# Performance work log

Hardware: AMD Instinct MI355X
Metric: run time of the kernel (lower is better)

The kernel has to match this reference:

```python
import jax, jax.numpy as jnp
import numpy as np

N_NODES = 100000
N_EDGES = 1600000
IN_DIM, HID_DIM, OUT_DIM = 128, 64, 64


def setup_inputs() -> dict:
    key = jax.random.key(0)
    ks = jax.random.split(key, 8)
    x = jax.random.normal(ks[0], (N_NODES, IN_DIM), dtype=jnp.float32)
    edge_index = jax.random.randint(ks[1], (2, N_EDGES), 0, N_NODES, dtype=jnp.int32)
    edge_weight = jax.random.uniform(ks[2], (N_EDGES,), dtype=jnp.float32)
    # GCNConv parameters (glorot-ish init)
    w1 = jax.random.normal(ks[3], (IN_DIM, HID_DIM), dtype=jnp.float32) / np.sqrt(IN_DIM)
    b1 = jnp.zeros((HID_DIM,), dtype=jnp.float32)
    w2 = jax.random.normal(ks[4], (HID_DIM, OUT_DIM), dtype=jnp.float32) / np.sqrt(HID_DIM)
    b2 = jnp.zeros((OUT_DIM,), dtype=jnp.float32)
    return {"x": x, "edge_index": edge_index, "edge_weight": edge_weight,
            "w1": w1, "b1": b1, "w2": w2, "b2": b2}


def _gcn_conv(h, src, dst, edge_weight, w, b, n_nodes):
    # GCNConv(normalize=False): linear transform, then edge-weighted scatter-add
    # (source_to_target flow: gather from src, scatter-sum into dst), then bias.
    h = h @ w                                   # [N, out]
    msg = h[src] * edge_weight[:, None]          # [E, out] irregular gather
    agg = jax.ops.segment_sum(msg, dst, num_segments=n_nodes)  # [N, out]
    return agg + b


def reference(x, edge_index, edge_weight, w1, b1, w2, b2):
    src, dst = edge_index[0], edge_index[1]
    n = x.shape[0]
    # Dropout is identity in eval mode (training=False).
    h = _gcn_conv(x, src, dst, edge_weight, w1, b1, n)
    h = jax.nn.relu(h)
    out = _gcn_conv(h, src, dst, edge_weight, w2, b2, n)
    return out
```

## Files before the change

### kernel.cpp

```cpp
#include <hip/hip_runtime.h>
#include <hip/hip_bf16.h>


#define N_NODES 100000
#define N_EDGES 1600000
#define NB1     391
#define T1      4096
#define NT1     391
#define CAP1    4706

typedef unsigned short ushort_t;
typedef unsigned int uint_t;
typedef __attribute__((ext_vector_type(8))) short bf16x8;
typedef __attribute__((ext_vector_type(4))) float floatx4;
typedef __attribute__((ext_vector_type(8))) ushort_t ushort8v;

static __device__ __forceinline__ float bf2f(ushort_t h) {
    return __uint_as_float(((uint_t)h) << 16);
}
static __device__ __forceinline__ ushort_t f2bf(float f) {
    uint_t u = __float_as_uint(f);
    u = (u + 0x7FFF + ((u >> 16) & 1)) >> 16;
    return (ushort_t)u;
}

__global__ __launch_bounds__(512) void k_init(int* __restrict__ gcursor)
{
    int t = threadIdx.x;
    if (t < NB1) gcursor[t] = t * CAP1;
}

__global__ __launch_bounds__(512) void k_pass1(
    const int* __restrict__ src, const int* __restrict__ dst,
    const float* __restrict__ ew, int* __restrict__ gcursor,
    int2* __restrict__ recs1, int E)
{
    __shared__ int cnt[NB1], start[NB1], cursor[NB1], gb[NB1];
    __shared__ int s[512];
    __shared__ int2 stg[T1];
    __shared__ ushort_t sb[T1];
    const int t = threadIdx.x, b = blockIdx.x;

    if (t < NB1) cnt[t] = 0;
    __syncthreads();
    const int e0 = b * T1;
    const int e1 = min(E, e0 + T1);
    for (int e = e0 + t; e < e1; e += 512)
        atomicAdd(&cnt[dst[e] >> 8], 1);
    __syncthreads();
    const int v = (t < NB1) ? cnt[t] : 0;
    s[t] = v;
    #pragma unroll
    for (int off = 1; off < 512; off <<= 1) {
        __syncthreads();
        int a = (t >= off) ? s[t - off] : 0;
        __syncthreads();
        s[t] += a;
    }
    __syncthreads();
    if (t < NB1) {
        int st = s[t] - v;
        start[t]  = st;
        cursor[t] = st;
        gb[t]     = atomicAdd(&gcursor[t], v);
    }
    __syncthreads();
    for (int e = e0 + t; e < e1; e += 512) {
        int d  = dst[e];
        int bk = d >> 8;
        int p  = atomicAdd(&cursor[bk], 1);
        int2 r;
        r.x = ((d & 255) << 17) | src[e];
        r.y = __float_as_int(ew[e]);
        stg[p] = r;
        sb[p]  = (ushort_t)bk;
    }
    __syncthreads();
    const int n = e1 - e0;
    for (int i = t; i < n; i += 512) {
        int bk = sb[i];
        recs1[gb[bk] + (i - start[bk])] = stg[i];
    }
}

__global__ __launch_bounds__(256) void k_pass2(
    const int2* __restrict__ recs1, const int* __restrict__ gcursor,
    int2* __restrict__ recs2, int2* __restrict__ nodeinfo, int N)
{
    __shared__ int cnt[256];
    __shared__ int s[256];
    __shared__ int cursor[256];
    const int t = threadIdx.x, b = blockIdx.x;
    const int lo = b * CAP1;
    const int hi = gcursor[b];

    cnt[t] = 0;
    __syncthreads();
    for (int j = lo + t; j < hi; j += 256)
        atomicAdd(&cnt[((uint_t)recs1[j].x) >> 17], 1);
    __syncthreads();
    const int v = cnt[t];
    s[t] = v;
    #pragma unroll
    for (int off = 1; off < 256; off <<= 1) {
        __syncthreads();
        int a = (t >= off) ? s[t - off] : 0;
        __syncthreads();
        s[t] += a;
    }
    __syncthreads();
    const int stl = s[t] - v;
    cursor[t] = stl;
    const int ng = b * 256 + t;
    if (ng < N) {
        int2 ni; ni.x = lo + stl; ni.y = v;
        nodeinfo[ng] = ni;
    }
    __syncthreads();
    for (int j = lo + t; j < hi; j += 256) {
        int2 r = recs1[j];
        int dl = ((uint_t)r.x) >> 17;
        int p  = atomicAdd(&cursor[dl], 1);
        int2 o;
        o.x = r.x & 0x1FFFF;
        o.y = r.y;
        recs2[lo + p] = o;
    }
}

__global__ __launch_bounds__(256) void k_gemm1(
    const float* __restrict__ X, const float* __restrict__ W,
    ushort_t* __restrict__ Y, int N)
{
    __shared__ ushort_t sA[64 * 136];
    __shared__ ushort_t sB[64 * 136];
    const int tid  = threadIdx.x;
    const int row0 = blockIdx.x * 64;

    for (int i = tid; i < 64 * 32; i += 256) {
        int r = i >> 5, c4 = (i & 31) * 4;
        int rg = row0 + r; if (rg > N - 1) rg = N - 1;
        float4 v = *(const float4*)(X + (size_t)rg * 128 + c4);
        ushort4 pk = make_ushort4(f2bf(v.x), f2bf(v.y), f2bf(v.z), f2bf(v.w));
        *(ushort4*)(sA + r * 136 + c4) = pk;
    }
    for (int i = tid; i < 128 * 16; i += 256) {
        int k = i >> 4, n4 = (i & 15) * 4;
        float4 v = *(const float4*)(W + (size_t)k * 64 + n4);
        sB[(n4 + 0) * 136 + k] = f2bf(v.x);
        sB[(n4 + 1) * 136 + k] = f2bf(v.y);
        sB[(n4 + 2) * 136 + k] = f2bf(v.z);
        sB[(n4 + 3) * 136 + k] = f2bf(v.w);
    }
    __syncthreads();

    const int wid = tid >> 6, lane = tid & 63;
    const int m = lane & 15, quad = lane >> 4;
    floatx4 acc[4] = {};

    #pragma unroll
    for (int ks = 0; ks < 4; ++ks) {
        bf16x8 a = *(const bf16x8*)(sA + (wid * 16 + m) * 136 + ks * 32 + quad * 8);
        #pragma unroll
        for (int nt = 0; nt < 4; ++nt) {
            bf16x8 bfr = *(const bf16x8*)(sB + (nt * 16 + m) * 136 + ks * 32 + quad * 8);
            acc[nt] = __builtin_amdgcn_mfma_f32_16x16x32_bf16(a, bfr, acc[nt], 0, 0, 0);
        }
    }
    __syncthreads();
    #pragma unroll
    for (int nt = 0; nt < 4; ++nt)
        #pragma unroll
        for (int r = 0; r < 4; ++r)
            sA[(wid * 16 + quad * 4 + r) * 72 + nt * 16 + m] = f2bf(acc[nt][r]);
    __syncthreads();
    for (int i = tid; i < 64 * 8; i += 256) {
        int rr = i >> 3, c8 = (i & 7) * 8;
        int rg = row0 + rr;
        if (rg < N)
            *(ushort8v*)(Y + (size_t)rg * 64 + c8) =
                *(const ushort8v*)(sA + rr * 72 + c8);
    }
}

__global__ __launch_bounds__(256) void k_gemm2(
    const ushort_t* __restrict__ X, const float* __restrict__ W,
    ushort_t* __restrict__ Y, int N)
{
    __shared__ ushort_t sA[64 * 72];
    __shared__ ushort_t sB[64 * 72];
    const int tid  = threadIdx.x;
    const int row0 = blockIdx.x * 64;

    for (int i = tid; i < 64 * 16; i += 256) {
        int r = i >> 4, c4 = (i & 15) * 4;
        int rg = row0 + r; if (rg > N - 1) rg = N - 1;
        *(ushort4*)(sA + r * 72 + c4) =
            *(const ushort4*)(X + (size_t)rg * 64 + c4);
    }
    for (int i = tid; i < 64 * 16; i += 256) {
        int k = i >> 4, n4 = (i & 15) * 4;
        float4 v = *(const float4*)(W + (size_t)k * 64 + n4);
        sB[(n4 + 0) * 72 + k] = f2bf(v.x);
        sB[(n4 + 1) * 72 + k] = f2bf(v.y);
        sB[(n4 + 2) * 72 + k] = f2bf(v.z);
        sB[(n4 + 3) * 72 + k] = f2bf(v.w);
    }
    __syncthreads();

    const int wid = tid >> 6, lane = tid & 63;
    const int m = lane & 15, quad = lane >> 4;
    floatx4 acc[4] = {};

    #pragma unroll
    for (int ks = 0; ks < 2; ++ks) {
        bf16x8 a = *(const bf16x8*)(sA + (wid * 16 + m) * 72 + ks * 32 + quad * 8);
        #pragma unroll
        for (int nt = 0; nt < 4; ++nt) {
            bf16x8 bfr = *(const bf16x8*)(sB + (nt * 16 + m) * 72 + ks * 32 + quad * 8);
            acc[nt] = __builtin_amdgcn_mfma_f32_16x16x32_bf16(a, bfr, acc[nt], 0, 0, 0);
        }
    }
    __syncthreads();
    #pragma unroll
    for (int nt = 0; nt < 4; ++nt)
        #pragma unroll
        for (int r = 0; r < 4; ++r)
            sA[(wid * 16 + quad * 4 + r) * 72 + nt * 16 + m] = f2bf(acc[nt][r]);
    __syncthreads();
    for (int i = tid; i < 64 * 8; i += 256) {
        int rr = i >> 3, c8 = (i & 7) * 8;
        int rg = row0 + rr;
        if (rg < N)
            *(ushort8v*)(Y + (size_t)rg * 64 + c8) =
                *(const ushort8v*)(sA + rr * 72 + c8);
    }
}

template<bool RELU, bool OUT_BF16>
__global__ __launch_bounds__(256) void k_gather(
    const ushort_t* __restrict__ H, const int2* __restrict__ recs,
    const int2* __restrict__ nodeinfo, const float* __restrict__ bias,
    void* __restrict__ out)
{
    const int wid  = threadIdx.x >> 6;
    const int lane = threadIdx.x & 63;
    const int n0   = (blockIdx.x * 4 + wid) * 2;
    const int n1   = n0 + 1;

    const int2 niA = nodeinfo[n0];
    const int2 niB = nodeinfo[n1];
    int baseA = niA.x; const int endA = niA.x + niA.y;
    int baseB = niB.x; const int endB = niB.x + niB.y;

    const int g  = lane >> 4;
    const int c4 = (lane & 15) * 4;

    float a0 = 0.f, a1 = 0.f, a2 = 0.f, a3 = 0.f;
    float b0 = 0.f, b1 = 0.f, b2 = 0.f, b3 = 0.f;

    while (baseA < endA || baseB < endB) {
        int mA = endA - baseA; if (mA > 64) mA = 64;
        int mB = endB - baseB; if (mB > 64) mB = 64;
        int2 rA = (mA > 0) ? recs[baseA + (lane < mA ? lane : mA - 1)]
                           : make_int2(0, 0);
        int2 rB = (mB > 0) ? recs[baseB + (lane < mB ? lane : mB - 1)]
                           : make_int2(0, 0);
        float wAf = __int_as_float(rA.y);
        float wBf = __int_as_float(rB.y);
        int mm = mA > mB ? mA : mB;
        #pragma unroll 2
        for (int jj = 0; jj < mm; jj += 4) {
            int idx = jj + g;
            int   sA = __shfl(rA.x, idx);
            float wA = __shfl(wAf, idx);
            int   sB = __shfl(rB.x, idx);
            float wB = __shfl(wBf, idx);
            if (idx >= mA) wA = 0.f;
            if (idx >= mB) wB = 0.f;
            ushort4 hA = *(const ushort4*)(H + (size_t)sA * 64 + c4);
            ushort4 hB = *(const ushort4*)(H + (size_t)sB * 64 + c4);
            a0 = fmaf(wA, bf2f(hA.x), a0);
            a1 = fmaf(wA, bf2f(hA.y), a1);
            a2 = fmaf(wA, bf2f(hA.z), a2);
            a3 = fmaf(wA, bf2f(hA.w), a3);
            b0 = fmaf(wB, bf2f(hB.x), b0);
            b1 = fmaf(wB, bf2f(hB.y), b1);
            b2 = fmaf(wB, bf2f(hB.z), b2);
            b3 = fmaf(wB, bf2f(hB.w), b3);
        }
        baseA += 64;
        baseB += 64;
    }
    a0 += __shfl_down(a0, 32); a1 += __shfl_down(a1, 32);
    a2 += __shfl_down(a2, 32); a3 += __shfl_down(a3, 32);
    b0 += __shfl_down(b0, 32); b1 += __shfl_down(b1, 32);
    b2 += __shfl_down(b2, 32); b3 += __shfl_down(b3, 32);
    a0 += __shfl_down(a0, 16); a1 += __shfl_down(a1, 16);
    a2 += __shfl_down(a2, 16); a3 += __shfl_down(a3, 16);
    b0 += __shfl_down(b0, 16); b1 += __shfl_down(b1, 16);
    b2 += __shfl_down(b2, 16); b3 += __shfl_down(b3, 16);

    if (lane < 16) {
        float4 bv = *(const float4*)(bias + c4);
        float vA0 = a0 + bv.x, vA1 = a1 + bv.y, vA2 = a2 + bv.z, vA3 = a3 + bv.w;
        float vB0 = b0 + bv.x, vB1 = b1 + bv.y, vB2 = b2 + bv.z, vB3 = b3 + bv.w;
        if (RELU) {
            vA0 = fmaxf(vA0, 0.f); vA1 = fmaxf(vA1, 0.f);
            vA2 = fmaxf(vA2, 0.f); vA3 = fmaxf(vA3, 0.f);
            vB0 = fmaxf(vB0, 0.f); vB1 = fmaxf(vB1, 0.f);
            vB2 = fmaxf(vB2, 0.f); vB3 = fmaxf(vB3, 0.f);
        }
        if (OUT_BF16) {
            *(ushort4*)((ushort_t*)out + (size_t)n0 * 64 + c4) =
                make_ushort4(f2bf(vA0), f2bf(vA1), f2bf(vA2), f2bf(vA3));
            *(ushort4*)((ushort_t*)out + (size_t)n1 * 64 + c4) =
                make_ushort4(f2bf(vB0), f2bf(vB1), f2bf(vB2), f2bf(vB3));
        } else {
            *(float4*)((float*)out + (size_t)n0 * 64 + c4) =
                make_float4(vA0, vA1, vA2, vA3);
            *(float4*)((float*)out + (size_t)n1 * 64 + c4) =
                make_float4(vB0, vB1, vB2, vB3);
        }
    }
}

extern "C" void kernel_launch(void* const* d_in, const int* in_sizes, int n_in,
                              void* d_out, int out_size, void* d_ws, size_t ws_size,
                              hipStream_t stream) {
    const float* x   = (const float*)d_in[0];
    const int*   ei  = (const int*)  d_in[1];
    const float* ew  = (const float*)d_in[2];
    const float* w1  = (const float*)d_in[3];
    const float* b1  = (const float*)d_in[4];
    const float* w2  = (const float*)d_in[5];
    const float* b2  = (const float*)d_in[6];
    float* out = (float*)d_out;

    const int N = N_NODES, E = N_EDGES;
    const int* src = ei;
    const int* dst = ei + E;

    char* p = (char*)d_ws;
    ushort_t* bufA   = (ushort_t*)p;  p += (size_t)N_NODES * 64 * 2;
    int2*     recs2  = (int2*)p;      p += (size_t)NB1 * CAP1 * 8;
    int2*     recs1  = (int2*)p;
    ushort_t* bufB   = (ushort_t*)p;  p += (size_t)NB1 * CAP1 * 8;
    int*      gcur   = (int*)p;       p += 2048;
    int2*     ninfo  = (int2*)p;      p += (size_t)N_NODES * 8;

    k_init <<<1, 512, 0, stream>>>(gcur);
    k_pass1<<<NT1, 512, 0, stream>>>(src, dst, ew, gcur, recs1, E);
    k_pass2<<<NB1, 256, 0, stream>>>(recs1, gcur, recs2, ninfo, N);

    k_gemm1<<<(N + 63) / 64, 256, 0, stream>>>(x, w1, bufA, N);
    k_gather<true, true><<<N / 8, 256, 0, stream>>>(bufA, recs2, ninfo, b1, bufB);

    k_gemm2<<<(N + 63) / 64, 256, 0, stream>>>(bufB, w2, bufA, N);
    k_gather<false, false><<<N / 8, 256, 0, stream>>>(bufA, recs2, ninfo, b2, out);
}
```

Measured before the change: 246.8 us.

## Merge edge bucketing pass1 with first GEMM into one launch; widen pass2 blocks

Pass1 (edge bucketing by destination) and the first feature GEMM are independent, so they now run in one launch. Blocks below NT1 do the bucketing, and the remaining blocks run a 128-row, 512-thread version of the GEMM, with both sharing one raw shared-memory buffer. The aim is to overlap the memory-bound sort with the GEMM and drop a launch. Separately, pass2 now uses 1024-thread blocks to scan the bucket records faster, and the gather inner loop is unrolled 4 instead of 2. The risks are the larger shared-memory footprint per block and the larger GEMM tile lowering occupancy.

```diff
diff --git a/kernel.cpp b/kernel.cpp
--- a/kernel.cpp
+++ b/kernel.cpp
@@ -8,6 +8,7 @@
 #define T1      4096
 #define NT1     391
 #define CAP1    4706
+#define GB1     782
 
 typedef unsigned short ushort_t;
 typedef unsigned int uint_t;
@@ -30,60 +31,120 @@
     if (t < NB1) gcursor[t] = t * CAP1;
 }
 
-__global__ __launch_bounds__(512) void k_pass1(
+__global__ __launch_bounds__(512) void k_p1g1(
     const int* __restrict__ src, const int* __restrict__ dst,
     const float* __restrict__ ew, int* __restrict__ gcursor,
-    int2* __restrict__ recs1, int E)
-{
-    __shared__ int cnt[NB1], start[NB1], cursor[NB1], gb[NB1];
-    __shared__ int s[512];
-    __shared__ int2 stg[T1];
-    __shared__ ushort_t sb[T1];
-    const int t = threadIdx.x, b = blockIdx.x;
-
-    if (t < NB1) cnt[t] = 0;
-    __syncthreads();
-    const int e0 = b * T1;
-    const int e1 = min(E, e0 + T1);
-    for (int e = e0 + t; e < e1; e += 512)
-        atomicAdd(&cnt[dst[e] >> 8], 1);
-    __syncthreads();
-    const int v = (t < NB1) ? cnt[t] : 0;
-    s[t] = v;
-    #pragma unroll
-    for (int off = 1; off < 512; off <<= 1) {
-        __syncthreads();
-        int a = (t >= off) ? s[t - off] : 0;
-        __syncthreads();
-        s[t] += a;
-    }
-    __syncthreads();
-    if (t < NB1) {
-        int st = s[t] - v;
-        start[t]  = st;
-        cursor[t] = st;
-        gb[t]     = atomicAdd(&gcursor[t], v);
-    }
-    __syncthreads();
-    for (int e = e0 + t; e < e1; e += 512) {
-        int d  = dst[e];
-        int bk = d >> 8;
-        int p  = atomicAdd(&cursor[bk], 1);
-        int2 r;
-        r.x = ((d & 255) << 17) | src[e];
-        r.y = __float_as_int(ew[e]);
-        stg[p] = r;
-        sb[p]  = (ushort_t)bk;
-    }
-    __syncthreads();
-    const int n = e1 - e0;
-    for (int i = t; i < n; i += 512) {
-        int bk = sb[i];
-        recs1[gb[bk] + (i - start[bk])] = stg[i];
-    }
-}
-
-__global__ __launch_bounds__(256) void k_pass2(
+    int2* __restrict__ recs1, int E,
+    const float* __restrict__ X, const float* __restrict__ W,
+    ushort_t* __restrict__ Y, int N)
+{
+    __shared__ __align__(16) char smem[52224];
+    const int tid = threadIdx.x;
+
+    if (blockIdx.x < NT1) {
+        int* cnt     = (int*)smem;
+        int* start   = cnt + NB1;
+        int* cursor  = start + NB1;
+        int* gb      = cursor + NB1;
+        int* s       = (int*)(smem + 6256);
+        int2* stg    = (int2*)(smem + 8304);
+        ushort_t* sb = (ushort_t*)(smem + 41072);
+        const int t = tid, b = blockIdx.x;
+
+        if (t < NB1) cnt[t] = 0;
+        __syncthreads();
+        const int e0 = b * T1;
+        const int e1 = min(E, e0 + T1);
+        for (int e = e0 + t; e < e1; e += 512)
+            atomicAdd(&cnt[dst[e] >> 8], 1);
+        __syncthreads();
+        const int v = (t < NB1) ? cnt[t] : 0;
+        s[t] = v;
+        #pragma unroll
+        for (int off = 1; off < 512; off <<= 1) {
+            __syncthreads();
+            int a = (t >= off) ? s[t - off] : 0;
+            __syncthreads();
+            s[t] += a;
+        }
+        __syncthreads();
+        if (t < NB1) {
+            int st = s[t] - v;
+            start[t]  = st;
+            cursor[t] = st;
+            gb[t]     = atomicAdd(&gcursor[t], v);
+        }
+        __syncthreads();
+        for (int e = e0 + t; e < e1; e += 512) {
+            int d  = dst[e];
+            int bk = d >> 8;
+            int p  = atomicAdd(&cursor[bk], 1);
+            int2 r;
+            r.x = ((d & 255) << 17) | src[e];
+            r.y = __float_as_int(ew[e]);
+            stg[p] = r;
+            sb[p]  = (ushort_t)bk;
+        }
+        __syncthreads();
+        const int n = e1 - e0;
+        for (int i = t; i < n; i += 512) {
+            int bk = sb[i];
+            recs1[gb[bk] + (i - start[bk])] = stg[i];
+        }
+    } else {
+        ushort_t* sA = (ushort_t*)smem;
+        ushort_t* sB = (ushort_t*)(smem + 34816);
+        const int b    = blockIdx.x - NT1;
+        const int row0 = b * 128;
+
+        for (int i = tid; i < 128 * 32; i += 512) {
+            int r = i >> 5, c4 = (i & 31) * 4;
+            int rg = row0 + r; if (rg > N - 1) rg = N - 1;
+            float4 v = *(const float4*)(X + (size_t)rg * 128 + c4);
+            ushort4 pk = make_ushort4(f2bf(v.x), f2bf(v.y), f2bf(v.z), f2bf(v.w));
+            *(ushort4*)(sA + r * 136 + c4) = pk;
+        }
+        for (int i = tid; i < 128 * 16; i += 512) {
+            int k = i >> 4, n4 = (i & 15) * 4;
+            float4 v = *(const float4*)(W + (size_t)k * 64 + n4);
+            sB[(n4 + 0) * 136 + k] = f2bf(v.x);
+            sB[(n4 + 1) * 136 + k] = f2bf(v.y);
+            sB[(n4 + 2) * 136 + k] = f2bf(v.z);
+            sB[(n4 + 3) * 136 + k] = f2bf(v.w);
+        }
+        __syncthreads();
+
+        const int wid = tid >> 6, lane = tid & 63;
+        const int m = lane & 15, quad = lane >> 4;
+        floatx4 acc[4] = {};
+
+        #pragma unroll
+        for (int ks = 0; ks < 4; ++ks) {
+            bf16x8 a = *(const bf16x8*)(sA + (wid * 16 + m) * 136 + ks * 32 + quad * 8);
+            #pragma unroll
+            for (int nt = 0; nt < 4; ++nt) {
+                bf16x8 bfr = *(const bf16x8*)(sB + (nt * 16 + m) * 136 + ks * 32 + quad * 8);
+                acc[nt] = __builtin_amdgcn_mfma_f32_16x16x32_bf16(a, bfr, acc[nt], 0, 0, 0);
+            }
+        }
+        __syncthreads();
+        #pragma unroll
+        for (int nt = 0; nt < 4; ++nt)
+            #pragma unroll
+            for (int r = 0; r < 4; ++r)
+                sA[(wid * 16 + quad * 4 + r) * 72 + nt * 16 + m] = f2bf(acc[nt][r]);
+        __syncthreads();
+        for (int i = tid; i < 128 * 8; i += 512) {
+            int rr = i >> 3, c8 = (i & 7) * 8;
+            int rg = row0 + rr;
+            if (rg < N)
+                *(ushort8v*)(Y + (size_t)rg * 64 + c8) =
+                    *(const ushort8v*)(sA + rr * 72 + c8);
+        }
+    }
+}
+
+__global__ __launch_bounds__(1024) void k_pass2(
     const int2* __restrict__ recs1, const int* __restrict__ gcursor,
     int2* __restrict__ recs2, int2* __restrict__ nodeinfo, int N)
 {
@@ -94,30 +155,32 @@
     const int lo = b * CAP1;
     const int hi = gcursor[b];
 
-    cnt[t] = 0;
-    __syncthreads();
-    for (int j = lo + t; j < hi; j += 256)
+    if (t < 256) cnt[t] = 0;
+    __syncthreads();
+    for (int j = lo + t; j < hi; j += 1024)
         atomicAdd(&cnt[((uint_t)recs1[j].x) >> 17], 1);
     __syncthreads();
-    const int v = cnt[t];
-    s[t] = v;
+    const int v = (t < 256) ? cnt[t] : 0;
+    if (t < 256) s[t] = v;
     #pragma unroll
     for (int off = 1; off < 256; off <<= 1) {
         __syncthreads();
-        int a = (t >= off) ? s[t - off] : 0;
-        __syncthreads();
-        s[t] += a;
-    }
-    __syncthreads();
-    const int stl = s[t] - v;
-    cursor[t] = stl;
-    const int ng = b * 256 + t;
-    if (ng < N) {
-        int2 ni; ni.x = lo + stl; ni.y = v;
-        nodeinfo[ng] = ni;
-    }
-    __syncthreads();
-    for (int j = lo + t; j < hi; j += 256) {
+        int a = (t >= off && t < 256) ? s[t - off] : 0;
+        __syncthreads();
+        if (t < 256) s[t] += a;
+    }
+    __syncthreads();
+    if (t < 256) {
+        const int stl = s[t] - v;
+        cursor[t] = stl;
+        const int ng = b * 256 + t;
+        if (ng < N) {
+            int2 ni; ni.x = lo + stl; ni.y = v;
+            nodeinfo[ng] = ni;
+        }
+    }
+    __syncthreads();
+    for (int j = lo + t; j < hi; j += 1024) {
         int2 r = recs1[j];
         int dl = ((uint_t)r.x) >> 17;
         int p  = atomicAdd(&cursor[dl], 1);
@@ -125,61 +188,6 @@
         o.x = r.x & 0x1FFFF;
         o.y = r.y;
         recs2[lo + p] = o;
-    }
-}
-
-__global__ __launch_bounds__(256) void k_gemm1(
-    const float* __restrict__ X, const float* __restrict__ W,
-    ushort_t* __restrict__ Y, int N)
-{
-    __shared__ ushort_t sA[64 * 136];
-    __shared__ ushort_t sB[64 * 136];
-    const int tid  = threadIdx.x;
-    const int row0 = blockIdx.x * 64;
-
-    for (int i = tid; i < 64 * 32; i += 256) {
-        int r = i >> 5, c4 = (i & 31) * 4;
-        int rg = row0 + r; if (rg > N - 1) rg = N - 1;
-        float4 v = *(const float4*)(X + (size_t)rg * 128 + c4);
-        ushort4 pk = make_ushort4(f2bf(v.x), f2bf(v.y), f2bf(v.z), f2bf(v.w));
-        *(ushort4*)(sA + r * 136 + c4) = pk;
-    }
-    for (int i = tid; i < 128 * 16; i += 256) {
-        int k = i >> 4, n4 = (i & 15) * 4;
-        float4 v = *(const float4*)(W + (size_t)k * 64 + n4);
-        sB[(n4 + 0) * 136 + k] = f2bf(v.x);
-        sB[(n4 + 1) * 136 + k] = f2bf(v.y);
-        sB[(n4 + 2) * 136 + k] = f2bf(v.z);
-        sB[(n4 + 3) * 136 + k] = f2bf(v.w);
-    }
-    __syncthreads();
-
-    const int wid = tid >> 6, lane = tid & 63;
-    const int m = lane & 15, quad = lane >> 4;
-    floatx4 acc[4] = {};
-
-    #pragma unroll
-    for (int ks = 0; ks < 4; ++ks) {
-        bf16x8 a = *(const bf16x8*)(sA + (wid * 16 + m) * 136 + ks * 32 + quad * 8);
-        #pragma unroll
-        for (int nt = 0; nt < 4; ++nt) {
-            bf16x8 bfr = *(const bf16x8*)(sB + (nt * 16 + m) * 136 + ks * 32 + quad * 8);
-            acc[nt] = __builtin_amdgcn_mfma_f32_16x16x32_bf16(a, bfr, acc[nt], 0, 0, 0);
-        }
-    }
-    __syncthreads();
-    #pragma unroll
-    for (int nt = 0; nt < 4; ++nt)
-        #pragma unroll
-        for (int r = 0; r < 4; ++r)
-            sA[(wid * 16 + quad * 4 + r) * 72 + nt * 16 + m] = f2bf(acc[nt][r]);
-    __syncthreads();
-    for (int i = tid; i < 64 * 8; i += 256) {
-        int rr = i >> 3, c8 = (i & 7) * 8;
-        int rg = row0 + rr;
-        if (rg < N)
-            *(ushort8v*)(Y + (size_t)rg * 64 + c8) =
-                *(const ushort8v*)(sA + rr * 72 + c8);
     }
 }
 
@@ -269,7 +277,7 @@
         float wAf = __int_as_float(rA.y);
         float wBf = __int_as_float(rB.y);
         int mm = mA > mB ? mA : mB;
-        #pragma unroll 2
+        #pragma unroll 4
         for (int jj = 0; jj < mm; jj += 4) {
             int idx = jj + g;
             int   sA = __shfl(rA.x, idx);
@@ -350,10 +358,10 @@
     int2*     ninfo  = (int2*)p;      p += (size_t)N_NODES * 8;
 
     k_init <<<1, 512, 0, stream>>>(gcur);
-    k_pass1<<<NT1, 512, 0, stream>>>(src, dst, ew, gcur, recs1, E);
-    k_pass2<<<NB1, 256, 0, stream>>>(recs1, gcur, recs2, ninfo, N);
-
-    k_gemm1<<<(N + 63) / 64, 256, 0, stream>>>(x, w1, bufA, N);
+    k_p1g1 <<<NT1 + GB1, 512, 0, stream>>>(src, dst, ew, gcur, recs1, E,
+                                           x, w1, bufA, N);
+    k_pass2<<<NB1, 1024, 0, stream>>>(recs1, gcur, recs2, ninfo, N);
+
     k_gather<true, true><<<N / 8, 256, 0, stream>>>(bufA, recs2, ninfo, b1, bufB);
 
     k_gemm2<<<(N + 63) / 64, 256, 0, stream>>>(bufB, w2, bufA, N);
```

Result: faster. 232.6 us (-5.7%).
